# Kernel tuning notes

Hardware: AMD Instinct MI355X
Metric: run time of the kernel (lower is better)

## Reference

```python
import jax, jax.numpy as jnp
import numpy as np

BLK = 64          # BLOCK_M == BLOCK_N == 64
TOPK_RATIO = 0.25


def _block_map(q, k, topk):
    # mean_pool of q blocks and mean-centered k blocks, then top-k key blocks per query block
    B, H, L, D = q.shape
    nb = L // BLK
    k_cent = k - jnp.mean(k, axis=-2, keepdims=True)
    pq = q.reshape(B, H, nb, BLK, D).mean(axis=3)          # [B,H,Mb,D]
    pk = k_cent.reshape(B, H, nb, BLK, D).mean(axis=3)     # [B,H,Nb,D]
    score = jnp.einsum('bhmd,bhnd->bhmn', pq, pk)
    _, lut = jax.lax.top_k(score, topk)                    # [B,H,Mb,topk] int32
    return lut


def reference(q, k, v):
    B, H, L, D = q.shape
    nb = L // BLK                       # M_BLOCKS == N_BLOCKS (L divisible by 64)
    topk = min(nb, int(TOPK_RATIO * nb))
    qk_scale = D ** (-0.5)

    lut = jax.lax.stop_gradient(_block_map(q, k, topk))    # routing is non-differentiable

    qb = q.reshape(B, H, nb, BLK, D)
    kb = k.reshape(B, H, nb, BLK, D)
    vb = v.reshape(B, H, nb, BLK, D)

    # gather selected key/value blocks per query block: [B,H,Mb,topk,BLK,D]
    idx = lut[:, :, :, :, None, None]
    k_sel = jnp.take_along_axis(kb[:, :, None], idx, axis=3)
    v_sel = jnp.take_along_axis(vb[:, :, None], idx, axis=3)

    # block-sparse attention restricted to the selected blocks
    s = jnp.einsum('bhmqd,bhmtkd->bhmqtk', qb, k_sel) * qk_scale
    s = s.reshape(B, H, nb, BLK, topk * BLK)
    p = jax.nn.softmax(s, axis=-1)                         # online-softmax equivalent
    v_flat = v_sel.reshape(B, H, nb, topk * BLK, D)
    o = jnp.einsum('bhmqn,bhmnd->bhmqd', p, v_flat)
    return o.reshape(B, H, L, D)


def setup_inputs() -> dict:
    key = jax.random.key(0)
    k1, k2, k3 = jax.random.split(key, 3)
    shape = (2, 8, 4096, 64)
    return {
        'q': jax.random.normal(k1, shape, dtype=jnp.float32),
        'k': jax.random.normal(k2, shape, dtype=jnp.float32),
        'v': jax.random.normal(k3, shape, dtype=jnp.float32),
    }
```

## Files before the change

### kernel.cpp

```cpp
#include <hip/hip_runtime.h>
#include <hip/hip_bf16.h>

#define B_ 2
#define H_ 8
#define L_ 4096
#define D_ 64
#define NB_ 64
#define TOPK_ 16
#define BH_ 16

typedef __bf16 bf16x8 __attribute__((ext_vector_type(8)));
typedef float f32x4 __attribute__((ext_vector_type(4)));

#if __has_builtin(__builtin_amdgcn_exp2f)
#define EXP2(x) __builtin_amdgcn_exp2f(x)
#else
#define EXP2(x) exp2f(x)
#endif

__device__ __forceinline__ void async_copy16(void* lds, const void* g) {
  __builtin_amdgcn_global_load_lds(
      (const __attribute__((address_space(1))) void*)g,
      (__attribute__((address_space(3))) void*)lds, 16, 0, 0);
}

__global__ __launch_bounds__(256) void prep_all_kernel(
    const float* __restrict__ q, const float* __restrict__ k,
    const float* __restrict__ v,
    float* __restrict__ pq, float* __restrict__ pk,
    __bf16* __restrict__ kswz, __bf16* __restrict__ vtswz) {
  const int tid = threadIdx.x;
  if (blockIdx.x < BH_ * NB_) {
    const int blk = blockIdx.x;
    const int bh = blk >> 6, m = blk & 63;
    const int d = tid & 63, g = tid >> 6;
    const float* qb = q + ((size_t)bh * L_ + m * 64 + g * 16) * D_ + d;
    float sq = 0.f;
#pragma unroll
    for (int i = 0; i < 16; i++) sq += qb[(size_t)i * D_];
    __shared__ float bufq[4][64];
    bufq[g][d] = sq;
    __syncthreads();
    if (g == 0) {
      float tq = bufq[0][d] + bufq[1][d] + bufq[2][d] + bufq[3][d];
      pq[(size_t)blk * 64 + d] = tq * (1.f / 64.f);
    }
  } else if (blockIdx.x < 2 * BH_ * NB_) {
    const int blk = blockIdx.x - BH_ * NB_;
    const int srow = tid >> 2;
    const int sc16 = (tid & 3) * 16;
    __shared__ __align__(16) float s_kf[64][64];

    const float* ks = k + (size_t)blk * 4096 + srow * 64 + sc16;
    float kf[16];
#pragma unroll
    for (int h = 0; h < 4; h++) {
      float4 t4 = *(const float4*)(ks + h * 4);
      kf[h * 4 + 0] = t4.x; kf[h * 4 + 1] = t4.y; kf[h * 4 + 2] = t4.z; kf[h * 4 + 3] = t4.w;
      *(float4*)&s_kf[srow][sc16 + h * 4] = t4;
    }

    __bf16* gk = kswz + (size_t)blk * 4096;
#pragma unroll
    for (int h = 0; h < 2; h++) {
      int c8 = (sc16 >> 3) + h;
      bf16x8 kw;
#pragma unroll
      for (int j = 0; j < 8; j++) kw[j] = (__bf16)kf[h * 8 + j];
      *(bf16x8*)(gk + srow * 64 + ((c8 ^ (srow & 7)) << 3)) = kw;
    }
    __syncthreads();

    const int d = tid & 63, g = tid >> 6;
    float sk = 0.f;
#pragma unroll
    for (int i = 0; i < 16; i++) sk += s_kf[g * 16 + i][d];
    __shared__ float bufk[4][64];
    bufk[g][d] = sk;
    __syncthreads();
    if (g == 0) {
      float tk = bufk[0][d] + bufk[1][d] + bufk[2][d] + bufk[3][d];
      pk[(size_t)blk * 64 + d] = tk * (1.f / 64.f);
    }
  } else {
    const int blk = blockIdx.x - 2 * BH_ * NB_;
    const int srow = tid >> 2;
    const int sc16 = (tid & 3) * 16;

    const float* vs = v + (size_t)blk * 4096 + srow * 64 + sc16;
    float vf[16];
#pragma unroll
    for (int h = 0; h < 4; h++) {
      float4 u4 = *(const float4*)(vs + h * 4);
      vf[h * 4 + 0] = u4.x; vf[h * 4 + 1] = u4.y; vf[h * 4 + 2] = u4.z; vf[h * 4 + 3] = u4.w;
    }

    const int kpos = (srow & 32) + ((srow >> 2) & 3) * 8 + ((srow >> 4) & 1) * 4 + (srow & 3);
    __shared__ __align__(16) __bf16 s_vt[4096];
#pragma unroll
    for (int i = 0; i < 16; i++) {
      int d = sc16 + i;
      s_vt[d * 64 + (kpos ^ ((d & 7) << 3))] = (__bf16)vf[i];
    }
    __syncthreads();
    __bf16* gv = vtswz + (size_t)blk * 4096;
    *(bf16x8*)(gv + tid * 8)        = *(const bf16x8*)(s_vt + tid * 8);
    *(bf16x8*)(gv + 2048 + tid * 8) = *(const bf16x8*)(s_vt + 2048 + tid * 8);
  }
}

__global__ __launch_bounds__(256) void blockmap_kernel(
    const float* __restrict__ pq, const float* __restrict__ pk,
    int* __restrict__ lut) {
  const int g = blockIdx.x;
  const int bh = g >> 2, q4 = g & 3;
  const int t = threadIdx.x;
  const int lane = t & 63, w = t >> 6;

  __shared__ float s_pk[64][65];
  __shared__ float s_km[64];
  __shared__ float s_pq[16][64];
  __shared__ float s_sc[4][64];

#pragma unroll
  for (int i = 0; i < 16; i++) {
    int idx = i * 256 + t;
    s_pk[idx >> 6][idx & 63] = pk[(size_t)bh * 4096 + idx];
  }
#pragma unroll
  for (int i = 0; i < 4; i++) {
    int idx = i * 256 + t;
    s_pq[idx >> 6][idx & 63] = pq[(size_t)bh * 4096 + q4 * 1024 + idx];
  }
  __syncthreads();
  if (t < 64) {
    float s = 0.f;
#pragma unroll 8
    for (int r = 0; r < 64; r++) s += s_pk[r][t];
    s_km[t] = s * (1.f / 64.f);
  }
  __syncthreads();

#pragma unroll
  for (int rr = 0; rr < 4; rr++) {
    const int row = w * 4 + rr;
    float sc = 0.f;
#pragma unroll 8
    for (int d2 = 0; d2 < 64; ++d2)
      sc += s_pq[row][d2] * (s_pk[lane][d2] - s_km[d2]);
    s_sc[w][lane] = sc;
    __syncthreads();
    int rank = 0;
#pragma unroll 8
    for (int j = 0; j < 64; j++) {
      float o = s_sc[w][j];
      rank += (o > sc) || (o == sc && j < lane);
    }
    if (rank < TOPK_)
      lut[((size_t)bh * 64 + q4 * 16 + row) * TOPK_ + rank] = lane;
    __syncthreads();
  }
}

__global__ __launch_bounds__(256) void sparse_attn_fast(
    const float* __restrict__ q, const __bf16* __restrict__ kswz,
    const __bf16* __restrict__ vtswz, const float* __restrict__ pq,
    const float* __restrict__ pk, float* __restrict__ out) {
  const int bid = blockIdx.x;
  const int blk = (bid & 7) * 128 + (bid >> 3);
  const int bh = blk >> 6, m = blk & 63;
  const int tid = threadIdx.x;
  const int lane = tid & 63;
  const int w = tid >> 6;
  const int l16 = lane & 15, lhi = lane >> 4;

  __shared__ __align__(16) __bf16 KV[2][8192];
  __shared__ float s_km[64];
  __shared__ float s_pqr[64];
  __shared__ float s_sc[64];
  __shared__ int s_lut[TOPK_];

  {
    float (*s_pk)[65] = (float(*)[65]) & KV[0][0];
    const float* pkb = pk + (size_t)bh * 4096;
#pragma unroll
    for (int i = 0; i < 16; i++) {
      int idx = i * 256 + tid;
      s_pk[idx >> 6][idx & 63] = pkb[idx];
    }
    if (tid < 64) s_pqr[tid] = pq[((size_t)bh * 64 + m) * 64 + tid];
    __syncthreads();
    if (tid < 64) {
      float s = 0.f;
#pragma unroll 8
      for (int r = 0; r < 64; r++) s += s_pk[r][tid];
      s_km[tid] = s * (1.f / 64.f);
    }
    __syncthreads();
    float sc = 0.f;
#pragma unroll 8
    for (int d2 = 0; d2 < 64; ++d2)
      sc += s_pqr[d2] * (s_pk[lane][d2] - s_km[d2]);
    s_sc[lane] = sc;
    __syncthreads();
    int rank = 0;
#pragma unroll 8
    for (int j = 0; j < 64; j++) {
      float o = s_sc[j];
      rank += (o > sc) || (o == sc && j < lane);
    }
    if (rank < TOPK_) s_lut[rank] = lane;
    __syncthreads();
  }

  const size_t base = (size_t)bh * L_ * D_;
  const __bf16* kimg = kswz + (size_t)bh * 64 * 4096;
  const __bf16* vbase = vtswz + (size_t)bh * 64 * 4096;

  const float QSC = 0.125f * 1.44269504088896340736f;
  bf16x8 qf[2];
  {
    const float* qrow = q + base + (size_t)(m * 64 + w * 16 + l16) * D_;
#pragma unroll
    for (int s = 0; s < 2; s++) {
      const float* p0 = qrow + s * 32 + lhi * 8;
      float4 a = *(const float4*)p0;
      float4 b = *(const float4*)(p0 + 4);
      bf16x8 f;
      f[0] = (__bf16)(a.x * QSC); f[1] = (__bf16)(a.y * QSC);
      f[2] = (__bf16)(a.z * QSC); f[3] = (__bf16)(a.w * QSC);
      f[4] = (__bf16)(b.x * QSC); f[5] = (__bf16)(b.y * QSC);
      f[6] = (__bf16)(b.z * QSC); f[7] = (__bf16)(b.w * QSC);
      qf[s] = f;
    }
  }

  f32x4 acc_o[4];
#pragma unroll
  for (int i = 0; i < 4; i++) acc_o[i] = (f32x4){0.f, 0.f, 0.f, 0.f};
  float l_run = 0.f;

  auto stage = [&](int b, int kb) {
    const __bf16* gk = kimg + (size_t)kb * 4096;
    const __bf16* gv = vbase + (size_t)kb * 4096;
    async_copy16(&KV[b][0 * 2048 + w * 512], gk + 0 * 2048 + tid * 8);
    async_copy16(&KV[b][1 * 2048 + w * 512], gk + 1 * 2048 + tid * 8);
    async_copy16(&KV[b][4096 + 0 * 2048 + w * 512], gv + 0 * 2048 + tid * 8);
    async_copy16(&KV[b][4096 + 1 * 2048 + w * 512], gv + 1 * 2048 + tid * 8);
  };

  stage(0, s_lut[0]);

  for (int it = 0; it < TOPK_; ++it) {
    const int cur = it & 1;
    if (it + 1 < TOPK_) {
      stage(cur ^ 1, s_lut[it + 1]);
      asm volatile("s_waitcnt vmcnt(4)" ::: "memory");
    } else {
      asm volatile("s_waitcnt vmcnt(0)" ::: "memory");
    }
    __builtin_amdgcn_s_barrier();
    __builtin_amdgcn_sched_barrier(0);

    const __bf16* Kl = &KV[cur][0];
    const __bf16* Vt = &KV[cur][4096];

    f32x4 accs[4];
#pragma unroll
    for (int x = 0; x < 4; x++) accs[x] = (f32x4){0.f, 0.f, 0.f, 0.f};
    __builtin_amdgcn_s_setprio(1);
#pragma unroll
    for (int ct = 0; ct < 4; ct++) {
      const int key = ct * 16 + l16;
#pragma unroll
      for (int s = 0; s < 2; s++) {
        const int c8 = s * 4 + lhi;
        bf16x8 bk = *(const bf16x8*)&Kl[key * 64 + ((c8 ^ (key & 7)) << 3)];
        accs[ct] = __builtin_amdgcn_mfma_f32_16x16x32_bf16(bk, qf[s], accs[ct], 0, 0, 0);
      }
    }
    __builtin_amdgcn_s_setprio(0);

    bf16x8 pa0, pa1;
    float ls0 = 0.f, ls1 = 0.f;
#pragma unroll
    for (int j = 0; j < 8; j++) {
      float e0 = EXP2(accs[(j >> 2)][j & 3]);
      float e1 = EXP2(accs[2 + (j >> 2)][j & 3]);
      pa0[j] = (__bf16)e0; pa1[j] = (__bf16)e1;
      ls0 += e0; ls1 += e1;
    }
    l_run += ls0 + ls1;

    __builtin_amdgcn_s_setprio(1);
#pragma unroll
    for (int s2 = 0; s2 < 2; s2++) {
      const int c8 = s2 * 4 + lhi;
      const bf16x8 pa = s2 ? pa1 : pa0;
#pragma unroll
      for (int ct2 = 0; ct2 < 4; ct2++) {
        const int d = ct2 * 16 + l16;
        bf16x8 bv = *(const bf16x8*)&Vt[d * 64 + ((c8 ^ (d & 7)) << 3)];
        acc_o[ct2] = __builtin_amdgcn_mfma_f32_16x16x32_bf16(pa, bv, acc_o[ct2], 0, 0, 0);
      }
    }
    __builtin_amdgcn_s_setprio(0);

    __builtin_amdgcn_s_barrier();
  }

  l_run += __shfl_xor(l_run, 16, 64);
  l_run += __shfl_xor(l_run, 32, 64);
  float rq[4];
#pragma unroll
  for (int r = 0; r < 4; r++)
    rq[r] = 1.f / __shfl(l_run, (lane & 48) | (lhi * 4 + r), 64);

  float* ob = out + base + (size_t)(m * 64 + w * 16) * D_;
#pragma unroll
  for (int ct2 = 0; ct2 < 4; ct2++) {
#pragma unroll
    for (int r = 0; r < 4; r++) {
      const int row = lhi * 4 + r, col = ct2 * 16 + l16;
      ob[(size_t)row * D_ + col] = acc_o[ct2][r] * rq[r];
    }
  }
}

__global__ __launch_bounds__(256) void block_means_kernel(
    const float* __restrict__ q, const float* __restrict__ k,
    float* __restrict__ pq, float* __restrict__ pk) {
  const int blk = blockIdx.x;
  const int bh = blk >> 6, m = blk & 63;
  const int d = threadIdx.x & 63, g = threadIdx.x >> 6;
  const float* qb = q + ((size_t)bh * L_ + m * 64 + g * 16) * D_ + d;
  const float* kb = k + ((size_t)bh * L_ + m * 64 + g * 16) * D_ + d;
  float sq = 0.f, sk = 0.f;
#pragma unroll
  for (int i = 0; i < 16; i++) { sq += qb[(size_t)i * D_]; sk += kb[(size_t)i * D_]; }
  __shared__ float bufq[4][64];
  __shared__ float bufk[4][64];
  bufq[g][d] = sq; bufk[g][d] = sk;
  __syncthreads();
  if (g == 0) {
    float tq = bufq[0][d] + bufq[1][d] + bufq[2][d] + bufq[3][d];
    float tk = bufk[0][d] + bufk[1][d] + bufk[2][d] + bufk[3][d];
    pq[(size_t)blk * 64 + d] = tq * (1.f / 64.f);
    pk[(size_t)blk * 64 + d] = tk * (1.f / 64.f);
  }
}

__global__ __launch_bounds__(256) void sparse_attn_slow(
    const float* __restrict__ q, const float* __restrict__ k,
    const float* __restrict__ v, const int* __restrict__ lut,
    float* __restrict__ out) {
  const int blk = blockIdx.x;
  const int bh = blk >> 6, m = blk & 63;
  const int tid = threadIdx.x;
  const int lane = tid & 63;
  const int w = tid >> 6;
  const int l16 = lane & 15, lhi = lane >> 4;

  __shared__ __align__(16) __bf16 Kl[64 * 64];
  __shared__ __align__(16) __bf16 Vt[64 * 64];
  __shared__ __align__(16) __bf16 Pl[4][16 * 64];

  const size_t base = (size_t)bh * L_ * D_;

  bf16x8 qf[2];
  {
    const float* qrow = q + base + (size_t)(m * 64 + w * 16 + l16) * D_;
#pragma unroll
    for (int s = 0; s < 2; s++) {
      const float* p0 = qrow + s * 32 + lhi * 8;
      float4 a = *(const float4*)p0;
      float4 b = *(const float4*)(p0 + 4);
      bf16x8 f;
      f[0] = (__bf16)(a.x * 0.125f); f[1] = (__bf16)(a.y * 0.125f);
      f[2] = (__bf16)(a.z * 0.125f); f[3] = (__bf16)(a.w * 0.125f);
      f[4] = (__bf16)(b.x * 0.125f); f[5] = (__bf16)(b.y * 0.125f);
      f[6] = (__bf16)(b.z * 0.125f); f[7] = (__bf16)(b.w * 0.125f);
      qf[s] = f;
    }
  }

  f32x4 acc_o[4];
#pragma unroll
  for (int i = 0; i < 4; i++) acc_o[i] = (f32x4){0.f, 0.f, 0.f, 0.f};
  float m_run[4] = {-__builtin_inff(), -__builtin_inff(), -__builtin_inff(), -__builtin_inff()};
  float l_run[4] = {0.f, 0.f, 0.f, 0.f};

  const int srow = tid >> 2;
  const int sc16 = (tid & 3) * 16;

  for (int it = 0; it < TOPK_; ++it) {
    const int kb = lut[(size_t)blk * TOPK_ + it];
    __syncthreads();
    {
      const float* ks = k + base + (size_t)(kb * 64 + srow) * D_ + sc16;
      const float* vs = v + base + (size_t)(kb * 64 + srow) * D_ + sc16;
      float kf[16], vf[16];
#pragma unroll
      for (int h = 0; h < 4; h++) {
        float4 t4 = *(const float4*)(ks + h * 4);
        kf[h * 4 + 0] = t4.x; kf[h * 4 + 1] = t4.y; kf[h * 4 + 2] = t4.z; kf[h * 4 + 3] = t4.w;
        float4 u4 = *(const float4*)(vs + h * 4);
        vf[h * 4 + 0] = u4.x; vf[h * 4 + 1] = u4.y; vf[h * 4 + 2] = u4.z; vf[h * 4 + 3] = u4.w;
      }
#pragma unroll
      for (int h = 0; h < 2; h++) {
        int c8 = (sc16 >> 3) + h;
        bf16x8 kw;
#pragma unroll
        for (int j = 0; j < 8; j++) kw[j] = (__bf16)kf[h * 8 + j];
        *(bf16x8*)&Kl[srow * 64 + ((c8 ^ (srow & 7)) << 3)] = kw;
      }
#pragma unroll
      for (int i = 0; i < 16; i++) {
        int d = sc16 + i;
        Vt[d * 64 + (srow ^ ((d & 7) << 3))] = (__bf16)vf[i];
      }
    }
    __syncthreads();

    f32x4 accs[4];
#pragma unroll
    for (int i = 0; i < 4; i++) accs[i] = (f32x4){0.f, 0.f, 0.f, 0.f};
#pragma unroll
    for (int ct = 0; ct < 4; ct++) {
      const int key = ct * 16 + l16;
#pragma unroll
      for (int s = 0; s < 2; s++) {
        const int c8 = s * 4 + lhi;
        bf16x8 bk = *(const bf16x8*)&Kl[key * 64 + ((c8 ^ (key & 7)) << 3)];
        accs[ct] = __builtin_amdgcn_mfma_f32_16x16x32_bf16(qf[s], bk, accs[ct], 0, 0, 0);
      }
    }

    float pvals[4][4];
#pragma unroll
    for (int r = 0; r < 4; r++) {
      float mx = fmaxf(fmaxf(accs[0][r], accs[1][r]), fmaxf(accs[2][r], accs[3][r]));
#pragma unroll
      for (int off = 1; off < 16; off <<= 1) mx = fmaxf(mx, __shfl_xor(mx, off, 64));
      const float mnew = fmaxf(m_run[r], mx);
      const float scale = __expf(m_run[r] - mnew);
      float rs = 0.f;
#pragma unroll
      for (int ct = 0; ct < 4; ct++) {
        float e = __expf(accs[ct][r] - mnew);
        pvals[ct][r] = e; rs += e;
      }
#pragma unroll
      for (int off = 1; off < 16; off <<= 1) rs += __shfl_xor(rs, off, 64);
      l_run[r] = l_run[r] * scale + rs;
      m_run[r] = mnew;
#pragma unroll
      for (int ct = 0; ct < 4; ct++) acc_o[ct][r] *= scale;
    }

#pragma unroll
    for (int ct = 0; ct < 4; ct++) {
#pragma unroll
      for (int r = 0; r < 4; r++) {
        const int row = lhi * 4 + r, col = ct * 16 + l16;
        Pl[w][row * 64 + (col ^ ((row & 7) << 3))] = (__bf16)pvals[ct][r];
      }
    }
#pragma unroll
    for (int s = 0; s < 2; s++) {
      const int c8 = s * 4 + lhi;
      bf16x8 pa = *(const bf16x8*)&Pl[w][l16 * 64 + ((c8 ^ (l16 & 7)) << 3)];
#pragma unroll
      for (int ct2 = 0; ct2 < 4; ct2++) {
        const int d = ct2 * 16 + l16;
        bf16x8 bv = *(const bf16x8*)&Vt[d * 64 + ((c8 ^ (d & 7)) << 3)];
        acc_o[ct2] = __builtin_amdgcn_mfma_f32_16x16x32_bf16(pa, bv, acc_o[ct2], 0, 0, 0);
      }
    }
  }

  float* ob = out + base + (size_t)(m * 64 + w * 16) * D_;
#pragma unroll
  for (int ct2 = 0; ct2 < 4; ct2++) {
#pragma unroll
    for (int r = 0; r < 4; r++) {
      const int row = lhi * 4 + r, col = ct2 * 16 + l16;
      ob[(size_t)row * D_ + col] = acc_o[ct2][r] / l_run[r];
    }
  }
}

extern "C" void kernel_launch(void* const* d_in, const int* in_sizes, int n_in,
                              void* d_out, int out_size, void* d_ws, size_t ws_size,
                              hipStream_t stream) {
  const float* q = (const float*)d_in[0];
  const float* k = (const float*)d_in[1];
  const float* v = (const float*)d_in[2];
  float* out = (float*)d_out;

  float* pq = (float*)d_ws;
  float* pk = pq + (size_t)BH_ * NB_ * D_;
  int*   lut = (int*)(pk + (size_t)BH_ * NB_ * D_);
  char*  extra = (char*)(lut + (size_t)BH_ * NB_ * TOPK_);
  __bf16* kswz = (__bf16*)extra;
  __bf16* vtswz = kswz + (size_t)BH_ * NB_ * 4096;

  const size_t needed = (size_t)((char*)(vtswz + (size_t)BH_ * NB_ * 4096) - (char*)d_ws);
  const bool fast = ws_size >= needed;

  if (fast) {
    hipLaunchKernelGGL(prep_all_kernel, dim3(3 * BH_ * NB_), dim3(256), 0, stream,
                       q, k, v, pq, pk, kswz, vtswz);
    hipLaunchKernelGGL(sparse_attn_fast, dim3(BH_ * NB_), dim3(256), 0, stream,
                       q, kswz, vtswz, pq, pk, out);
  } else {
    hipLaunchKernelGGL(block_means_kernel, dim3(BH_ * NB_), dim3(256), 0, stream, q, k, pq, pk);
    hipLaunchKernelGGL(blockmap_kernel, dim3(BH_ * 4), dim3(256), 0, stream, pq, pk, lut);
    hipLaunchKernelGGL(sparse_attn_slow, dim3(BH_ * NB_), dim3(256), 0, stream, q, k, v, lut, out);
  }
}
```

Before: 48.21 us.

## Fuse query block-mean pooling into attention kernel and pack shared memory

```diff
diff --git a/kernel.cpp b/kernel.cpp
--- a/kernel.cpp
+++ b/kernel.cpp
@@ -25,28 +25,12 @@
 }
 
 __global__ __launch_bounds__(256) void prep_all_kernel(
-    const float* __restrict__ q, const float* __restrict__ k,
-    const float* __restrict__ v,
-    float* __restrict__ pq, float* __restrict__ pk,
+    const float* __restrict__ k, const float* __restrict__ v,
+    float* __restrict__ pk,
     __bf16* __restrict__ kswz, __bf16* __restrict__ vtswz) {
   const int tid = threadIdx.x;
   if (blockIdx.x < BH_ * NB_) {
     const int blk = blockIdx.x;
-    const int bh = blk >> 6, m = blk & 63;
-    const int d = tid & 63, g = tid >> 6;
-    const float* qb = q + ((size_t)bh * L_ + m * 64 + g * 16) * D_ + d;
-    float sq = 0.f;
-#pragma unroll
-    for (int i = 0; i < 16; i++) sq += qb[(size_t)i * D_];
-    __shared__ float bufq[4][64];
-    bufq[g][d] = sq;
-    __syncthreads();
-    if (g == 0) {
-      float tq = bufq[0][d] + bufq[1][d] + bufq[2][d] + bufq[3][d];
-      pq[(size_t)blk * 64 + d] = tq * (1.f / 64.f);
-    }
-  } else if (blockIdx.x < 2 * BH_ * NB_) {
-    const int blk = blockIdx.x - BH_ * NB_;
     const int srow = tid >> 2;
     const int sc16 = (tid & 3) * 16;
     __shared__ __align__(16) float s_kf[64][64];
@@ -83,7 +67,7 @@
       pk[(size_t)blk * 64 + d] = tk * (1.f / 64.f);
     }
   } else {
-    const int blk = blockIdx.x - 2 * BH_ * NB_;
+    const int blk = blockIdx.x - BH_ * NB_;
     const int srow = tid >> 2;
     const int sc16 = (tid & 3) * 16;
 
@@ -162,10 +146,10 @@
   }
 }
 
-__global__ __launch_bounds__(256) void sparse_attn_fast(
+__global__ __launch_bounds__(256, 5) void sparse_attn_fast(
     const float* __restrict__ q, const __bf16* __restrict__ kswz,
-    const __bf16* __restrict__ vtswz, const float* __restrict__ pq,
-    const float* __restrict__ pk, float* __restrict__ out) {
+    const __bf16* __restrict__ vtswz, const float* __restrict__ pk,
+    float* __restrict__ out) {
   const int bid = blockIdx.x;
   const int blk = (bid & 7) * 128 + (bid >> 3);
   const int bh = blk >> 6, m = blk & 63;
@@ -174,21 +158,48 @@
   const int w = tid >> 6;
   const int l16 = lane & 15, lhi = lane >> 4;
 
-  __shared__ __align__(16) __bf16 KV[2][8192];
-  __shared__ float s_km[64];
-  __shared__ float s_pqr[64];
-  __shared__ float s_sc[64];
-  __shared__ int s_lut[TOPK_];
+  __shared__ __align__(16) char smem[32768];
+  __bf16 (*KV)[8192] = reinterpret_cast<__bf16(*)[8192]>(smem);
+  float (*s_qf)[68] = reinterpret_cast<float(*)[68]>(smem);
+  float* bufq  = reinterpret_cast<float*>(smem + 17408);
+  float (*s_pk)[65] = reinterpret_cast<float(*)[65]>(smem);
+  float* s_pqr = reinterpret_cast<float*>(smem + 16640);
+  float* s_km  = reinterpret_cast<float*>(smem + 16896);
+  float* s_sc  = reinterpret_cast<float*>(smem + 17152);
+  int*   s_lut = reinterpret_cast<int*>(smem + 18432);
+
+  const size_t base = (size_t)bh * L_ * D_;
 
   {
-    float (*s_pk)[65] = (float(*)[65]) & KV[0][0];
+    const float* qsrc = q + base + (size_t)(m * 64) * D_;
+    const int r = tid >> 2, c = (tid & 3) * 16;
+    const float* qs = qsrc + r * 64 + c;
+#pragma unroll
+    for (int h = 0; h < 4; h++)
+      *(float4*)&s_qf[r][c + h * 4] = *(const float4*)(qs + h * 4);
+  }
+  __syncthreads();
+  {
+    const int d = tid & 63, g = tid >> 6;
+    float sq = 0.f;
+#pragma unroll
+    for (int i = 0; i < 16; i++) sq += s_qf[g * 16 + i][d];
+    bufq[g * 64 + d] = sq;
+  }
+  __syncthreads();
+  if (tid < 64) {
+    float tq = bufq[0 * 64 + tid] + bufq[1 * 64 + tid] + bufq[2 * 64 + tid] + bufq[3 * 64 + tid];
+    s_pqr[tid] = tq * (1.f / 64.f);
+  }
+  __syncthreads();
+
+  {
     const float* pkb = pk + (size_t)bh * 4096;
 #pragma unroll
     for (int i = 0; i < 16; i++) {
       int idx = i * 256 + tid;
       s_pk[idx >> 6][idx & 63] = pkb[idx];
     }
-    if (tid < 64) s_pqr[tid] = pq[((size_t)bh * 64 + m) * 64 + tid];
     __syncthreads();
     if (tid < 64) {
       float s = 0.f;
@@ -212,10 +223,22 @@
     if (rank < TOPK_) s_lut[rank] = lane;
     __syncthreads();
   }
-
-  const size_t base = (size_t)bh * L_ * D_;
+  const int myk = s_lut[lane & 15];
+  __syncthreads();
+
   const __bf16* kimg = kswz + (size_t)bh * 64 * 4096;
   const __bf16* vbase = vtswz + (size_t)bh * 64 * 4096;
+
+  auto stage = [&](int b, int kb) {
+    const __bf16* gk = kimg + (size_t)kb * 4096;
+    const __bf16* gv = vbase + (size_t)kb * 4096;
+    async_copy16(&KV[b][0 * 2048 + w * 512], gk + 0 * 2048 + tid * 8);
+    async_copy16(&KV[b][1 * 2048 + w * 512], gk + 1 * 2048 + tid * 8);
+    async_copy16(&KV[b][4096 + 0 * 2048 + w * 512], gv + 0 * 2048 + tid * 8);
+    async_copy16(&KV[b][4096 + 1 * 2048 + w * 512], gv + 1 * 2048 + tid * 8);
+  };
+
+  stage(0, __shfl(myk, 0, 64));
 
   const float QSC = 0.125f * 1.44269504088896340736f;
   bf16x8 qf[2];
@@ -240,21 +263,10 @@
   for (int i = 0; i < 4; i++) acc_o[i] = (f32x4){0.f, 0.f, 0.f, 0.f};
   float l_run = 0.f;
 
-  auto stage = [&](int b, int kb) {
-    const __bf16* gk = kimg + (size_t)kb * 4096;
-    const __bf16* gv = vbase + (size_t)kb * 4096;
-    async_copy16(&KV[b][0 * 2048 + w * 512], gk + 0 * 2048 + tid * 8);
-    async_copy16(&KV[b][1 * 2048 + w * 512], gk + 1 * 2048 + tid * 8);
-    async_copy16(&KV[b][4096 + 0 * 2048 + w * 512], gv + 0 * 2048 + tid * 8);
-    async_copy16(&KV[b][4096 + 1 * 2048 + w * 512], gv + 1 * 2048 + tid * 8);
-  };
-
-  stage(0, s_lut[0]);
-
   for (int it = 0; it < TOPK_; ++it) {
     const int cur = it & 1;
     if (it + 1 < TOPK_) {
-      stage(cur ^ 1, s_lut[it + 1]);
+      stage(cur ^ 1, __shfl(myk, it + 1, 64));
       asm volatile("s_waitcnt vmcnt(4)" ::: "memory");
     } else {
       asm volatile("s_waitcnt vmcnt(0)" ::: "memory");
@@ -510,10 +522,10 @@
   const bool fast = ws_size >= needed;
 
   if (fast) {
-    hipLaunchKernelGGL(prep_all_kernel, dim3(3 * BH_ * NB_), dim3(256), 0, stream,
-                       q, k, v, pq, pk, kswz, vtswz);
+    hipLaunchKernelGGL(prep_all_kernel, dim3(2 * BH_ * NB_), dim3(256), 0, stream,
+                       k, v, pk, kswz, vtswz);
     hipLaunchKernelGGL(sparse_attn_fast, dim3(BH_ * NB_), dim3(256), 0, stream,
-                       q, kswz, vtswz, pq, pk, out);
+                       q, kswz, vtswz, pk, out);
   } else {
     hipLaunchKernelGGL(block_means_kernel, dim3(BH_ * NB_), dim3(256), 0, stream, q, k, pq, pk);
     hipLaunchKernelGGL(blockmap_kernel, dim3(BH_ * 4), dim3(256), 0, stream, pq, pk, lut);
```

Result: faster. 44.28 us (-8.1%).
